# Performance work log

Measured on AMD Instinct MI355X. Metric: run time of the kernel, lower is better.

## Reference

```python
import jax, jax.numpy as jnp
import numpy as np

N, C, L, NUM_LAYERS = 512, 32, 1024, 3
BN_EPS = 1e-5


def setup_inputs() -> dict:
    key = jax.random.key(0)
    kx, kw, kb, kg, kbe = jax.random.split(key, 5)
    x = jax.random.normal(kx, (N, C, L), dtype=jnp.float32)
    # Per-channel, per-layer Linear weights: (C, num_layers, L_out, L_in)
    W = jax.random.normal(kw, (C, NUM_LAYERS, L, L), dtype=jnp.float32) / np.float32(np.sqrt(L))
    b = 0.01 * jax.random.normal(kb, (C, NUM_LAYERS, L), dtype=jnp.float32)
    # BatchNorm affine params for the num_layers-1 inner BN layers
    gamma = 1.0 + 0.1 * jax.random.normal(kg, (C, NUM_LAYERS - 1, L), dtype=jnp.float32)
    beta = 0.1 * jax.random.normal(kbe, (C, NUM_LAYERS - 1, L), dtype=jnp.float32)
    return {"x": x, "W": W, "b": b, "gamma": gamma, "beta": beta}


def reference(x, W, b, gamma, beta):
    """Fused per-channel MLP head.

    x: (N, C, L). For each channel c, applies num_layers Linear layers with
    ReLU + BatchNorm1d (training-mode batch stats, biased variance) between
    layers. All C channels computed as one batched GEMM per layer.
    """
    h = x
    for i in range(NUM_LAYERS):
        # batched per-channel Linear: (N,C,Lin) x (C,Lout,Lin) -> (N,C,Lout)
        h = jnp.einsum('ncl,cml->ncm', h, W[:, i]) + b[:, i][None]
        if i < NUM_LAYERS - 1:
            h = jax.nn.relu(h)
            # BatchNorm1d over the batch dim N, per (channel, feature)
            mean = jnp.mean(h, axis=0)          # (C, L)
            var = jnp.var(h, axis=0)            # biased variance, matches torch BN
            h = (h - mean) * jax.lax.rsqrt(var + BN_EPS) * gamma[:, i] + beta[:, i]
    return h
```

## Files before the change

kernel.cpp:

```cpp
#include <hip/hip_runtime.h>
#include <hip/hip_bf16.h>

#define NB 512
#define CCH 32
#define LF 1024
#define CL (CCH * LF)
#define BN_EPS 1e-5f

typedef __bf16 bf16x8 __attribute__((ext_vector_type(8)));
typedef float f32x4 __attribute__((ext_vector_type(4)));

__device__ __forceinline__ void gload16(const __bf16* g, __bf16* l) {
  __builtin_amdgcn_global_load_lds(
      (const __attribute__((address_space(1))) unsigned int*)g,
      (__attribute__((address_space(3))) unsigned int*)l, 16, 0, 0);
}

__global__ __launch_bounds__(256) void cvt_bf16(const float* __restrict__ s,
                                                __bf16* __restrict__ d) {
  const size_t i = ((size_t)blockIdx.x * 256 + threadIdx.x) * 8;
  f32x4 a = *(const f32x4*)(s + i);
  f32x4 b = *(const f32x4*)(s + i + 4);
  bf16x8 o = {(__bf16)a.x, (__bf16)a.y, (__bf16)a.z, (__bf16)a.w,
              (__bf16)b.x, (__bf16)b.y, (__bf16)b.z, (__bf16)b.w};
  *(bf16x8*)(d + i) = o;
}

template <bool RELU, bool BF16OUT>
__global__ __launch_bounds__(256, 3) void gemm_dma(
    const __bf16* __restrict__ Abf, const __bf16* __restrict__ Wall,
    const float* __restrict__ ball, void* __restrict__ outv, int layer) {
  __shared__ __bf16 As[4096];
  __shared__ __bf16 Bs[4096];

  const int tid = threadIdx.x;
  const int c = blockIdx.y;
  const int mtile = blockIdx.x & 3;
  const int ntile = blockIdx.x >> 2;
  const int m0 = mtile * 128, n0 = ntile * 128;

  const __bf16* A = Abf + (size_t)c * LF;
  const __bf16* Wp = Wall + (size_t)(c * 3 + layer) * LF * LF;
  const float* bias = ball + (size_t)(c * 3 + layer) * LF;

  const int lane = tid & 63;
  const int wv = tid >> 6;
  const int wm = (wv & 1) * 64;
  const int wn = (wv >> 1) * 64;
  const int l15 = lane & 15;
  const int quad = lane >> 4;

  const __bf16 *pa[2], *pb[2];
  __bf16 *la[2], *lb[2];
#pragma unroll
  for (int j = 0; j < 2; ++j) {
    const int s = wv * 128 + j * 64 + lane;
    const int q = s >> 7, r = s & 127;
    pa[j] = A + (size_t)(m0 + r) * CL + q * 8;
    pb[j] = Wp + (size_t)(n0 + r) * LF + q * 8;
    la[j] = As + (wv * 128 + j * 64) * 8;
    lb[j] = Bs + (wv * 128 + j * 64) * 8;
  }

  f32x4 acc[4][4] = {};

  for (int kt = 0; kt < LF / 32; ++kt) {
#pragma unroll
    for (int j = 0; j < 2; ++j) {
      gload16(pa[j], la[j]);
      gload16(pb[j], lb[j]);
      pa[j] += 32;
      pb[j] += 32;
    }
    __syncthreads();

    bf16x8 af[4], bfr[4];
#pragma unroll
    for (int mi = 0; mi < 4; ++mi)
      af[mi] = *(const bf16x8*)&As[(quad * 128 + wm + mi * 16 + l15) * 8];
#pragma unroll
    for (int ni = 0; ni < 4; ++ni)
      bfr[ni] = *(const bf16x8*)&Bs[(quad * 128 + wn + ni * 16 + l15) * 8];
#pragma unroll
    for (int mi = 0; mi < 4; ++mi)
#pragma unroll
      for (int ni = 0; ni < 4; ++ni)
        acc[mi][ni] = __builtin_amdgcn_mfma_f32_16x16x32_bf16(
            af[mi], bfr[ni], acc[mi][ni], 0, 0, 0);
    __syncthreads();
  }

#pragma unroll
  for (int ni = 0; ni < 4; ++ni) {
    const int feat = n0 + wn + ni * 16 + l15;
    const float bv = bias[feat];
#pragma unroll
    for (int mi = 0; mi < 4; ++mi) {
      const int row0 = m0 + wm + mi * 16 + quad * 4;
#pragma unroll
      for (int r = 0; r < 4; ++r) {
        float v = acc[mi][ni][r] + bv;
        if (RELU) v = fmaxf(v, 0.f);
        if (BF16OUT)
          ((__bf16*)outv)[(size_t)c * LF + (size_t)(row0 + r) * CL + feat] =
              (__bf16)v;
        else
          ((float*)outv)[(size_t)c * LF + (size_t)(row0 + r) * CL + feat] = v;
      }
    }
  }
}

__global__ __launch_bounds__(256, 4) void bn_fused(__bf16* __restrict__ H,
                                                   const float* __restrict__ gam,
                                                   const float* __restrict__ bet,
                                                   int bnl) {
  __shared__ float ssum[256], ssq[256], sscale[64], sshift[64];
  const int tid = threadIdx.x;
  const int f = tid & 63, g = tid >> 6;
  const int c = blockIdx.y;
  const int l = blockIdx.x * 64 + f;
  __bf16* col = H + (size_t)c * LF + l;

  float sum = 0.f, sq = 0.f;
  for (int n = g; n < NB; n += 4) {
    float v = (float)col[(size_t)n * CL];
    sum += v;
    sq += v * v;
  }
  ssum[tid] = sum;
  ssq[tid] = sq;
  __syncthreads();
  if (tid < 64) {
    sum = ssum[f] + ssum[64 + f] + ssum[128 + f] + ssum[192 + f];
    sq = ssq[f] + ssq[64 + f] + ssq[128 + f] + ssq[192 + f];
    const float mean = sum * (1.f / NB);
    const float var = sq * (1.f / NB) - mean * mean;
    const float rstd = rsqrtf(var + BN_EPS);
    const float sc = rstd * gam[(size_t)(c * 2 + bnl) * LF + l];
    sscale[f] = sc;
    sshift[f] = bet[(size_t)(c * 2 + bnl) * LF + l] - mean * sc;
  }
  __syncthreads();
  const float sc = sscale[f], sh = sshift[f];
  for (int n = g; n < NB; n += 4) {
    float v = (float)col[(size_t)n * CL];
    col[(size_t)n * CL] = (__bf16)(v * sc + sh);
  }
}

extern "C" void kernel_launch(void* const* d_in, const int* in_sizes, int n_in,
                              void* d_out, int out_size, void* d_ws,
                              size_t ws_size, hipStream_t stream) {
  const float* x = (const float*)d_in[0];
  const float* W = (const float*)d_in[1];
  const float* b = (const float*)d_in[2];
  const float* gamma = (const float*)d_in[3];
  const float* beta = (const float*)d_in[4];
  float* out = (float*)d_out;

  __bf16* Wbf = (__bf16*)d_ws;
  __bf16* xbf = Wbf + (size_t)CCH * 3 * LF * LF;
  __bf16* h1 = xbf + (size_t)NB * CL;
  __bf16* h2 = h1 + (size_t)NB * CL;

  const dim3 blk(256);
  const dim3 ggrid(32, CCH);
  const dim3 bgrid(16, CCH);

  cvt_bf16<<<dim3((CCH * 3 * LF * LF) / (8 * 256)), blk, 0, stream>>>(W, Wbf);
  cvt_bf16<<<dim3(((size_t)NB * CL) / (8 * 256)), blk, 0, stream>>>(x, xbf);

  gemm_dma<true, true><<<ggrid, blk, 0, stream>>>(xbf, Wbf, b, h1, 0);
  bn_fused<<<bgrid, blk, 0, stream>>>(h1, gamma, beta, 0);
  gemm_dma<true, true><<<ggrid, blk, 0, stream>>>(h1, Wbf, b, h2, 1);
  bn_fused<<<bgrid, blk, 0, stream>>>(h2, gamma, beta, 1);
  gemm_dma<false, false><<<ggrid, blk, 0, stream>>>(h2, Wbf, b, out, 2);
}
```

Baseline: 980.9 us.

## Pre-swizzle weights into tile images and store activations channel-major

Weight conversion now writes each 128-row by 32-k tile already in the LDS layout, so GEMM weight loads become fully contiguous 4096-element blocks. Activations are transposed to a (C, N, L) layout so each channel's rows are contiguous with stride L instead of C*L. Block index mapping is changed so the 8 n-tiles sharing an A m-tile run adjacently, improving L2 reuse of A. The cost is a heavier weight-conversion kernel that stages through shared memory, and an x conversion that also transposes.

After: 957.7 us. 2.4% less time.

```diff
diff --git a/kernel.cpp b/kernel.cpp
--- a/kernel.cpp
+++ b/kernel.cpp
@@ -8,6 +8,7 @@
 #define BN_EPS 1e-5f
 
 typedef __bf16 bf16x8 __attribute__((ext_vector_type(8)));
+typedef __bf16 bf16x4 __attribute__((ext_vector_type(4)));
 typedef float f32x4 __attribute__((ext_vector_type(4)));
 
 __device__ __forceinline__ void gload16(const __bf16* g, __bf16* l) {
@@ -16,31 +17,56 @@
       (__attribute__((address_space(3))) unsigned int*)l, 16, 0, 0);
 }
 
-__global__ __launch_bounds__(256) void cvt_bf16(const float* __restrict__ s,
-                                                __bf16* __restrict__ d) {
-  const size_t i = ((size_t)blockIdx.x * 256 + threadIdx.x) * 8;
-  f32x4 a = *(const f32x4*)(s + i);
-  f32x4 b = *(const f32x4*)(s + i + 4);
-  bf16x8 o = {(__bf16)a.x, (__bf16)a.y, (__bf16)a.z, (__bf16)a.w,
-              (__bf16)b.x, (__bf16)b.y, (__bf16)b.z, (__bf16)b.w};
-  *(bf16x8*)(d + i) = o;
+__global__ __launch_bounds__(256) void cvt_w(const float* __restrict__ W,
+                                             __bf16* __restrict__ Wswz) {
+  __shared__ __bf16 img[4096];
+  const int tid = threadIdx.x;
+  const int bid = blockIdx.x;
+  const int n0 = (bid & 7) * 128;
+  const float* Wr = W + (size_t)(bid >> 3) * LF * LF;
+  __bf16* dst = Wswz + (size_t)bid * 131072;
+  const int sr = tid >> 3, kseg = tid & 7;
+  const int q = kseg >> 1, bsub = (kseg & 1) * 4;
+  for (int kt = 0; kt < 32; ++kt) {
+    const int k0 = kt * 32 + kseg * 4;
+#pragma unroll
+    for (int i = 0; i < 4; ++i) {
+      const int r = i * 32 + sr;
+      f32x4 v = *(const f32x4*)(Wr + (size_t)(n0 + r) * LF + k0);
+      bf16x4 o = {(__bf16)v.x, (__bf16)v.y, (__bf16)v.z, (__bf16)v.w};
+      *(bf16x4*)&img[(q * 128 + r) * 8 + bsub] = o;
+    }
+    __syncthreads();
+    *(bf16x8*)(dst + kt * 4096 + tid * 16) = *(bf16x8*)&img[tid * 16];
+    *(bf16x8*)(dst + kt * 4096 + tid * 16 + 8) = *(bf16x8*)&img[tid * 16 + 8];
+    __syncthreads();
+  }
+}
+
+__global__ __launch_bounds__(256) void cvt_x(const float* __restrict__ x,
+                                             __bf16* __restrict__ hA) {
+  const int n = blockIdx.x, c = blockIdx.y;
+  const float* src = x + ((size_t)n * CCH + c) * LF + threadIdx.x * 4;
+  __bf16* dst = hA + ((size_t)c * NB + n) * LF + threadIdx.x * 4;
+  f32x4 v = *(const f32x4*)src;
+  bf16x4 o = {(__bf16)v.x, (__bf16)v.y, (__bf16)v.z, (__bf16)v.w};
+  *(bf16x4*)dst = o;
 }
 
 template <bool RELU, bool BF16OUT>
 __global__ __launch_bounds__(256, 3) void gemm_dma(
-    const __bf16* __restrict__ Abf, const __bf16* __restrict__ Wall,
+    const __bf16* __restrict__ Abf, const __bf16* __restrict__ Wswz,
     const float* __restrict__ ball, void* __restrict__ outv, int layer) {
   __shared__ __bf16 As[4096];
   __shared__ __bf16 Bs[4096];
 
   const int tid = threadIdx.x;
   const int c = blockIdx.y;
-  const int mtile = blockIdx.x & 3;
-  const int ntile = blockIdx.x >> 2;
+  const int mtile = blockIdx.x >> 3;
+  const int ntile = blockIdx.x & 7;
   const int m0 = mtile * 128, n0 = ntile * 128;
 
-  const __bf16* A = Abf + (size_t)c * LF;
-  const __bf16* Wp = Wall + (size_t)(c * 3 + layer) * LF * LF;
+  const __bf16* A = Abf + (size_t)c * NB * LF;
   const float* bias = ball + (size_t)(c * 3 + layer) * LF;
 
   const int lane = tid & 63;
@@ -56,21 +82,21 @@
   for (int j = 0; j < 2; ++j) {
     const int s = wv * 128 + j * 64 + lane;
     const int q = s >> 7, r = s & 127;
-    pa[j] = A + (size_t)(m0 + r) * CL + q * 8;
-    pb[j] = Wp + (size_t)(n0 + r) * LF + q * 8;
+    pa[j] = A + (size_t)(m0 + r) * LF + q * 8;
+    pb[j] = Wswz + (size_t)((c * 3 + layer) * 8 + ntile) * 131072 + s * 8;
     la[j] = As + (wv * 128 + j * 64) * 8;
     lb[j] = Bs + (wv * 128 + j * 64) * 8;
   }
 
   f32x4 acc[4][4] = {};
 
-  for (int kt = 0; kt < LF / 32; ++kt) {
+  for (int kt = 0; kt < 32; ++kt) {
 #pragma unroll
     for (int j = 0; j < 2; ++j) {
       gload16(pa[j], la[j]);
       gload16(pb[j], lb[j]);
       pa[j] += 32;
-      pb[j] += 32;
+      pb[j] += 4096;
     }
     __syncthreads();
 
@@ -102,10 +128,9 @@
         float v = acc[mi][ni][r] + bv;
         if (RELU) v = fmaxf(v, 0.f);
         if (BF16OUT)
-          ((__bf16*)outv)[(size_t)c * LF + (size_t)(row0 + r) * CL + feat] =
-              (__bf16)v;
+          ((__bf16*)outv)[((size_t)c * NB + row0 + r) * LF + feat] = (__bf16)v;
         else
-          ((float*)outv)[(size_t)c * LF + (size_t)(row0 + r) * CL + feat] = v;
+          ((float*)outv)[((size_t)(row0 + r) * CCH + c) * LF + feat] = v;
       }
     }
   }
@@ -120,11 +145,11 @@
   const int f = tid & 63, g = tid >> 6;
   const int c = blockIdx.y;
   const int l = blockIdx.x * 64 + f;
-  __bf16* col = H + (size_t)c * LF + l;
+  __bf16* col = H + (size_t)c * NB * LF + l;
 
   float sum = 0.f, sq = 0.f;
   for (int n = g; n < NB; n += 4) {
-    float v = (float)col[(size_t)n * CL];
+    float v = (float)col[(size_t)n * LF];
     sum += v;
     sq += v * v;
   }
@@ -144,8 +169,8 @@
   __syncthreads();
   const float sc = sscale[f], sh = sshift[f];
   for (int n = g; n < NB; n += 4) {
-    float v = (float)col[(size_t)n * CL];
-    col[(size_t)n * CL] = (__bf16)(v * sc + sh);
+    float v = (float)col[(size_t)n * LF];
+    col[(size_t)n * LF] = (__bf16)(v * sc + sh);
   }
 }
 
@@ -159,8 +184,8 @@
   const float* beta = (const float*)d_in[4];
   float* out = (float*)d_out;
 
-  __bf16* Wbf = (__bf16*)d_ws;
-  __bf16* xbf = Wbf + (size_t)CCH * 3 * LF * LF;
+  __bf16* Wswz = (__bf16*)d_ws;
+  __bf16* xbf = Wswz + (size_t)CCH * 3 * LF * LF;
   __bf16* h1 = xbf + (size_t)NB * CL;
   __bf16* h2 = h1 + (size_t)NB * CL;
 
@@ -168,12 +193,12 @@
   const dim3 ggrid(32, CCH);
   const dim3 bgrid(16, CCH);
 
-  cvt_bf16<<<dim3((CCH * 3 * LF * LF) / (8 * 256)), blk, 0, stream>>>(W, Wbf);
-  cvt_bf16<<<dim3(((size_t)NB * CL) / (8 * 256)), blk, 0, stream>>>(x, xbf);
-
-  gemm_dma<true, true><<<ggrid, blk, 0, stream>>>(xbf, Wbf, b, h1, 0);
+  cvt_w<<<dim3(CCH * 3 * 8), blk, 0, stream>>>(W, Wswz);
+  cvt_x<<<dim3(NB, CCH), blk, 0, stream>>>(x, xbf);
+
+  gemm_dma<true, true><<<ggrid, blk, 0, stream>>>(xbf, Wswz, b, h1, 0);
   bn_fused<<<bgrid, blk, 0, stream>>>(h1, gamma, beta, 0);
-  gemm_dma<true, true><<<ggrid, blk, 0, stream>>>(h1, Wbf, b, h2, 1);
+  gemm_dma<true, true><<<ggrid, blk, 0, stream>>>(h1, Wswz, b, h2, 1);
   bn_fused<<<bgrid, blk, 0, stream>>>(h2, gamma, beta, 1);
-  gemm_dma<false, false><<<ggrid, blk, 0, stream>>>(h2, Wbf, b, out, 2);
-}
+  gemm_dma<false, false><<<ggrid, blk, 0, stream>>>(h2, Wswz, b, out, 2);
+}
```
